# Kernel optimization log

Hardware: AMD Instinct MI355X
Metric: run time of the kernel (lower is better)

The kernel has to match this reference:

```python
import jax, jax.numpy as jnp
import numpy as np

SCALE_X = 3.0 ** 0.5  # sqrt(1 + 2*exp(highway_bias)) with highway_bias=0, rescale=True


def setup_inputs() -> dict:
    key = jax.random.key(0)
    k1, k2, k3 = jax.random.split(key, 3)
    L, B, d = 1024, 32, 512
    x = jax.random.normal(k1, (L, B, d), dtype=jnp.float32)
    # weight [n_in, 3*n_out]; scaled like xavier uniform range sqrt(3/d)
    weight = jax.random.normal(k2, (d, 3 * d), dtype=jnp.float32) * (1.0 / d) ** 0.5
    weight_c = jax.random.normal(k3, (2 * d,), dtype=jnp.float32) * 0.5
    bias = jnp.zeros((2 * d,), dtype=jnp.float32)
    c0 = jnp.zeros((B, d), dtype=jnp.float32)
    return {"x": x, "weight": weight, "weight_c": weight_c, "bias": bias, "c0": c0}


def reference(x, weight, weight_c, bias, c0):
    # x: [L, B, n_in], weight: [n_in, 3*n_out], weight_c/bias: [2*n_out], c0: [B, n_out]
    L, B, d_in = x.shape
    d = c0.shape[-1]
    # input projection GEMM: u[t,b,:] = x[t,b,:] @ W, split into (x_tilde, f_in, r_in)
    u = jnp.einsum('lbi,ik->lbk', x, weight).reshape(L, B, 3, d)
    vf, vr = weight_c[:d], weight_c[d:]
    bf, br = bias[:d], bias[d:]

    def step(c, inp):
        u_t, x_t = inp                                   # u_t: [B,3,d], x_t: [B,d]
        f = jax.nn.sigmoid(u_t[:, 1] + vf * c + bf)      # forget gate from c_{t-1}
        c_new = f * c + (1.0 - f) * u_t[:, 0]            # cell state
        r = jax.nn.sigmoid(u_t[:, 2] + vr * c_new + br)  # reset/highway gate from c_t
        g = jnp.tanh(c_new)                              # activation_type=1 (tanh)
        h = r * g + (1.0 - r) * (x_t * SCALE_X)          # highway skip (k=3: uses x*scale)
        return c_new, h

    c_last, h = jax.lax.scan(step, c0, (u, x))
    return h, c_last
```

## Files before the change

### kernel.cpp

```cpp
#include <hip/hip_runtime.h>
#include <hip/hip_bf16.h>


typedef __attribute__((ext_vector_type(8))) __bf16 bf16x8;
typedef __attribute__((ext_vector_type(4))) __bf16 bf16x4;
typedef __attribute__((ext_vector_type(4))) float floatx4;

#define WAITV(N) asm volatile("s_waitcnt vmcnt(" #N ")" ::: "memory")
#define WAITL() asm volatile("s_waitcnt lgkmcnt(0)" ::: "memory")

#define GK 512
#define GN 1536

__global__ __launch_bounds__(256) void cvt_w(const float* __restrict__ w,
                                             __bf16* __restrict__ wt) {
  __shared__ float tile[64][65];
  const int bk = blockIdx.x;
  const int bn = blockIdx.y;
  const int t = threadIdx.x;
  const int tr = t >> 6;
  const int tc = t & 63;
#pragma unroll
  for (int i = 0; i < 16; ++i) {
    int kl = i * 4 + tr;
    tile[kl][tc] = w[(size_t)(bk * 64 + kl) * GN + bn * 64 + tc];
  }
  __syncthreads();
#pragma unroll
  for (int i = 0; i < 16; ++i) {
    int nl = i * 4 + tr;
    wt[(size_t)(bn * 64 + nl) * GK + bk * 64 + tc] = (__bf16)tile[tc][nl];
  }
}

__global__ __launch_bounds__(512, 2) void fused_kernel(
    const float* __restrict__ x, const __bf16* __restrict__ wt,
    const float* __restrict__ wc, const float* __restrict__ bias,
    const float* __restrict__ c0, float* __restrict__ out) {
  __shared__ __attribute__((aligned(16))) __bf16 xbuf[2][16 * 512];
  __shared__ __attribute__((aligned(16))) float ubuf[2][16][201];
  const int g = blockIdx.x;
  const int b = (g & 7) * 4 + ((g >> 3) & 3);
  const int j0 = (g >> 5) * 64;
  const int wave = threadIdx.x >> 6;
  const int lane = threadIdx.x & 63;
  const int quad = lane >> 4, l16 = lane & 15;

  if (wave < 6) {
    const int comp = wave >> 1, hn = wave & 1;
    const int lnb = comp * 64 + hn * 32;
    const int nb = comp * 512 + j0 + hn * 32;
    bf16x8 breg[16][2];
#pragma unroll
    for (int ki = 0; ki < 16; ++ki)
#pragma unroll
      for (int nt = 0; nt < 2; ++nt)
        breg[ki][nt] = *(const bf16x8*)(wt + (size_t)(nb + nt * 16 + l16) * GK +
                                        ki * 32 + quad * 8);
    __builtin_amdgcn_s_barrier();
    for (int s = 0; s < 64; ++s) {
      const __bf16* xb = xbuf[s & 1];
      floatx4 acc0 = {}, acc1 = {};
#pragma unroll
      for (int ki = 0; ki < 16; ++ki) {
        bf16x8 af = *(const bf16x8*)(xb + l16 * 512 +
                                     (((4 * ki + quad) ^ (l16 & 7)) * 8));
        acc0 = __builtin_amdgcn_mfma_f32_16x16x32_bf16(af, breg[ki][0], acc0, 0, 0, 0);
        acc1 = __builtin_amdgcn_mfma_f32_16x16x32_bf16(af, breg[ki][1], acc1, 0, 0, 0);
      }
      float* ub = &ubuf[s & 1][0][0];
#pragma unroll
      for (int i = 0; i < 4; ++i) {
        ub[(quad * 4 + i) * 201 + lnb + l16] = acc0[i];
        ub[(quad * 4 + i) * 201 + lnb + 16 + l16] = acc1[i];
      }
      WAITL();
      __builtin_amdgcn_s_barrier();
    }
  } else if (wave == 6) {
    const float* xsrc = x + (size_t)b * 512;
    float4 xr[32];
#define XISSUE(BLK)                                                         \
  _Pragma("unroll") for (int v = 0; v < 32; ++v) {                          \
    int r = v >> 1;                                                         \
    int fq = (v & 1) * 64 + lane;                                           \
    xr[v] = *(const float4*)(xsrc + (size_t)((BLK) * 16 + r) * 16384 + fq * 4); \
  }
#define XWRITE(BUF)                                                         \
  _Pragma("unroll") for (int v = 0; v < 32; ++v) {                          \
    int r = v >> 1;                                                         \
    int fq = (v & 1) * 64 + lane;                                           \
    float4 w4 = xr[v];                                                      \
    bf16x4 o = {(__bf16)w4.x, (__bf16)w4.y, (__bf16)w4.z, (__bf16)w4.w};    \
    *(bf16x4*)((__bf16*)xbuf[BUF] + r * 512 + (((fq >> 1) ^ (r & 7)) * 8) + \
               (fq & 1) * 4) = o;                                           \
  }
    XISSUE(0);
    WAITV(0);
    XWRITE(0);
    XISSUE(1);
    WAITL();
    __builtin_amdgcn_s_barrier();
    for (int s = 0; s < 64; ++s) {
      if (s + 1 < 64) {
        WAITV(0);
        XWRITE((s + 1) & 1);
      }
      if (s + 2 < 64) XISSUE(s + 2);
      WAITL();
      __builtin_amdgcn_s_barrier();
    }
#undef XISSUE
#undef XWRITE
  } else {
    const int ob = b * 512 + j0 + lane;
    const float L2E = 1.4426950408889634f;
    const float vf = wc[j0 + lane], vr = wc[512 + j0 + lane];
    const float bfv = bias[j0 + lane], brv = bias[512 + j0 + lane];
    const float wf2 = -vf * L2E;
    const float wr2 = -vr * L2E;
    float c = c0[ob];
    float* op = out + ob;
    const float* xs2 = x + ob;
    float xa[16], xb2[16];
#define XLOAD(BANK, BLK)                                                    \
  _Pragma("unroll") for (int i = 0; i < 16; ++i) BANK[i] =                  \
      xs2[(size_t)((BLK) * 16 + i) * 16384];
#define CONSUME(S1, BANK)                                                   \
  {                                                                         \
    const float* ub = &ubuf[(S1) & 1][0][0];                                \
    float u0a[16], k2a[16], cc[16];                                         \
                        \
    _Pragma("unroll") for (int i = 0; i < 16; ++i) {                        \
      u0a[i] = ub[i * 201 + lane];                                          \
      float u1 = ub[i * 201 + 64 + lane];                                   \
      k2a[i] = -(u1 + bfv) * L2E;                                           \
    }                                                                       \
        \
    _Pragma("unroll") for (int i = 0; i < 16; ++i) {                        \
      float t = __builtin_fmaf(wf2, c, k2a[i]);                             \
      float e;                                                              \
      asm("v_exp_f32 %0, %1" : "=v"(e) : "v"(t));                           \
      float fr = __builtin_amdgcn_rcpf(1.f + e);                            \
      c = __builtin_fmaf(c - u0a[i], fr, u0a[i]);                           \
      cc[i] = c;                                                            \
    }                                                                       \
                \
    _Pragma("unroll") for (int i = 0; i < 16; ++i) {                        \
      float ci = cc[i];                                                     \
      float u2 = ub[i * 201 + 128 + lane];                                  \
      float t2 = __builtin_fmaf(wr2, ci, -(u2 + brv) * L2E);                \
      float e2;                                                             \
      asm("v_exp_f32 %0, %1" : "=v"(e2) : "v"(t2));                         \
      float rg = __builtin_amdgcn_rcpf(1.f + e2);                           \
      float t3 = __builtin_fabsf(ci) * (-2.f * L2E);                        \
      float e3;                                                             \
      asm("v_exp_f32 %0, %1" : "=v"(e3) : "v"(t3));                         \
      float gg = (1.f - e3) * __builtin_amdgcn_rcpf(1.f + e3);              \
      gg = __builtin_copysignf(gg, ci);                                     \
      float xsc = BANK[i] * 1.7320508075688772f;                            \
      float h = __builtin_fmaf(rg, gg - xsc, xsc);                          \
      op[(size_t)((S1) * 16 + i) * 16384] = h;                              \
    }                                                                       \
  }
    __builtin_amdgcn_s_barrier();
    XLOAD(xa, 0);
    __builtin_amdgcn_s_barrier();
    for (int sp = 1; sp < 63; sp += 2) {
      XLOAD(xb2, sp);
      WAITV(16);
      CONSUME(sp - 1, xa);
      __builtin_amdgcn_s_barrier();
      XLOAD(xa, sp + 1);
      WAITV(16);
      CONSUME(sp, xb2);
      __builtin_amdgcn_s_barrier();
    }
    XLOAD(xb2, 63);
    WAITV(16);
    CONSUME(62, xa);
    __builtin_amdgcn_s_barrier();
    WAITV(16);
    CONSUME(63, xb2);
    out[(size_t)16777216 + ob] = c;
#undef XLOAD
#undef CONSUME
  }
}

extern "C" void kernel_launch(void* const* d_in, const int* in_sizes, int n_in,
                              void* d_out, int out_size, void* d_ws, size_t ws_size,
                              hipStream_t stream) {
  const float* x = (const float*)d_in[0];
  const float* w = (const float*)d_in[1];
  const float* wc = (const float*)d_in[2];
  const float* bias = (const float*)d_in[3];
  const float* c0 = (const float*)d_in[4];
  float* out = (float*)d_out;

  char* ws = (char*)d_ws;
  __bf16* wt = (__bf16*)ws;

  cvt_w<<<dim3(8, 24), 256, 0, stream>>>(w, wt);
  fused_kernel<<<256, 512, 0, stream>>>(x, wt, wc, bias, c0, out);
}
```

Baseline: 204.0 us.

## Split recurrence into c-chain and output waves with three-stage pipeline

Each block shrinks from 8 to 6 waves: 3 MFMA waves, each computing 64 columns of one gate component, 1 x-loader wave, a new wave that runs only the serial c recurrence, and a final wave that computes the r gate, tanh and output from c values passed through a new LDS buffer. The u buffer becomes triple-buffered and the loop runs 66 stages, so GEMM, the c recurrence and the output stage overlap across consecutive 16-step chunks. This aims to take the exp, tanh and store work off the serial dependency chain and to allow 3 blocks per CU. In exchange it adds pipeline fill latency and LDS traffic, and doubles the B-fragment registers held by each MFMA wave.

```diff
diff --git a/kernel.cpp b/kernel.cpp
--- a/kernel.cpp
+++ b/kernel.cpp
@@ -33,51 +33,58 @@
   }
 }
 
-__global__ __launch_bounds__(512, 2) void fused_kernel(
+__global__ __launch_bounds__(384, 3) void fused_kernel(
     const float* __restrict__ x, const __bf16* __restrict__ wt,
     const float* __restrict__ wc, const float* __restrict__ bias,
     const float* __restrict__ c0, float* __restrict__ out) {
   __shared__ __attribute__((aligned(16))) __bf16 xbuf[2][16 * 512];
-  __shared__ __attribute__((aligned(16))) float ubuf[2][16][201];
+  __shared__ __attribute__((aligned(16))) float ubuf[3][16][194];
+  __shared__ __attribute__((aligned(16))) float ccbuf[2][16][64];
   const int g = blockIdx.x;
   const int b = (g & 7) * 4 + ((g >> 3) & 3);
   const int j0 = (g >> 5) * 64;
   const int wave = threadIdx.x >> 6;
   const int lane = threadIdx.x & 63;
   const int quad = lane >> 4, l16 = lane & 15;
-
-  if (wave < 6) {
-    const int comp = wave >> 1, hn = wave & 1;
-    const int lnb = comp * 64 + hn * 32;
-    const int nb = comp * 512 + j0 + hn * 32;
-    bf16x8 breg[16][2];
+  const float L2E = 1.4426950408889634f;
+
+  if (wave < 3) {
+    const int nb = wave * 512 + j0;
+    const int lnb = wave * 64;
+    bf16x8 breg[16][4];
 #pragma unroll
     for (int ki = 0; ki < 16; ++ki)
 #pragma unroll
-      for (int nt = 0; nt < 2; ++nt)
+      for (int nt = 0; nt < 4; ++nt)
         breg[ki][nt] = *(const bf16x8*)(wt + (size_t)(nb + nt * 16 + l16) * GK +
                                         ki * 32 + quad * 8);
     __builtin_amdgcn_s_barrier();
-    for (int s = 0; s < 64; ++s) {
-      const __bf16* xb = xbuf[s & 1];
-      floatx4 acc0 = {}, acc1 = {};
-#pragma unroll
-      for (int ki = 0; ki < 16; ++ki) {
-        bf16x8 af = *(const bf16x8*)(xb + l16 * 512 +
-                                     (((4 * ki + quad) ^ (l16 & 7)) * 8));
-        acc0 = __builtin_amdgcn_mfma_f32_16x16x32_bf16(af, breg[ki][0], acc0, 0, 0, 0);
-        acc1 = __builtin_amdgcn_mfma_f32_16x16x32_bf16(af, breg[ki][1], acc1, 0, 0, 0);
-      }
-      float* ub = &ubuf[s & 1][0][0];
-#pragma unroll
-      for (int i = 0; i < 4; ++i) {
-        ub[(quad * 4 + i) * 201 + lnb + l16] = acc0[i];
-        ub[(quad * 4 + i) * 201 + lnb + 16 + l16] = acc1[i];
+    int pu = 0;
+    for (int s = 0; s < 66; ++s) {
+      if (s < 64) {
+        const __bf16* xb = xbuf[s & 1];
+        floatx4 acc[4] = {};
+#pragma unroll
+        for (int ki = 0; ki < 16; ++ki) {
+          bf16x8 af = *(const bf16x8*)(xb + l16 * 512 +
+                                       (((4 * ki + quad) ^ (l16 & 7)) * 8));
+#pragma unroll
+          for (int nt = 0; nt < 4; ++nt)
+            acc[nt] = __builtin_amdgcn_mfma_f32_16x16x32_bf16(af, breg[ki][nt],
+                                                              acc[nt], 0, 0, 0);
+        }
+        float* ub = &ubuf[pu][0][0];
+#pragma unroll
+        for (int nt = 0; nt < 4; ++nt)
+#pragma unroll
+          for (int i = 0; i < 4; ++i)
+            ub[(quad * 4 + i) * 194 + lnb + nt * 16 + l16] = acc[nt][i];
+        pu = (pu == 2) ? 0 : pu + 1;
       }
       WAITL();
       __builtin_amdgcn_s_barrier();
     }
-  } else if (wave == 6) {
+  } else if (wave == 3) {
     const float* xsrc = x + (size_t)b * 512;
     float4 xr[32];
 #define XISSUE(BLK)                                                         \
@@ -101,7 +108,7 @@
     XISSUE(1);
     WAITL();
     __builtin_amdgcn_s_barrier();
-    for (int s = 0; s < 64; ++s) {
+    for (int s = 0; s < 66; ++s) {
       if (s + 1 < 64) {
         WAITV(0);
         XWRITE((s + 1) & 1);
@@ -112,43 +119,60 @@
     }
 #undef XISSUE
 #undef XWRITE
+  } else if (wave == 4) {
+    const int ob = b * 512 + j0 + lane;
+    const float vf = wc[j0 + lane], bfv = bias[j0 + lane];
+    const float wf2 = -vf * L2E;
+    float c = c0[ob];
+    __builtin_amdgcn_s_barrier();
+    int q = 0;
+    for (int s = 0; s < 66; ++s) {
+      if (s >= 1 && s <= 64) {
+        const float* ub = &ubuf[q][0][0];
+        float u0a[16], k2a[16];
+#pragma unroll
+        for (int i = 0; i < 16; ++i) {
+          u0a[i] = ub[i * 194 + lane];
+          k2a[i] = -(ub[i * 194 + 64 + lane] + bfv) * L2E;
+        }
+#pragma unroll
+        for (int i = 0; i < 16; ++i)
+          asm volatile("" : "+v"(u0a[i]), "+v"(k2a[i]));
+        __builtin_amdgcn_sched_barrier(0);
+        float* cb = &ccbuf[(s - 1) & 1][0][0];
+#pragma unroll
+        for (int i = 0; i < 16; ++i) {
+          float t = __builtin_fmaf(wf2, c, k2a[i]);
+          float e;
+          asm("v_exp_f32 %0, %1" : "=v"(e) : "v"(t));
+          float fr = __builtin_amdgcn_rcpf(1.f + e);
+          c = __builtin_fmaf(c - u0a[i], fr, u0a[i]);
+          cb[i * 64 + lane] = c;
+        }
+        q = (q == 2) ? 0 : q + 1;
+      }
+      WAITL();
+      __builtin_amdgcn_s_barrier();
+    }
   } else {
     const int ob = b * 512 + j0 + lane;
-    const float L2E = 1.4426950408889634f;
-    const float vf = wc[j0 + lane], vr = wc[512 + j0 + lane];
-    const float bfv = bias[j0 + lane], brv = bias[512 + j0 + lane];
-    const float wf2 = -vf * L2E;
+    const float vr = wc[512 + j0 + lane], brv = bias[512 + j0 + lane];
     const float wr2 = -vr * L2E;
-    float c = c0[ob];
     float* op = out + ob;
     const float* xs2 = x + ob;
-    float xa[16], xb2[16];
-#define XLOAD(BANK, BLK)                                                    \
+    float xA[16], xB[16];
+    int qp = 0;
+    __builtin_amdgcn_s_barrier();
+#define XLOADP(BANK, BLK)                                                   \
   _Pragma("unroll") for (int i = 0; i < 16; ++i) BANK[i] =                  \
       xs2[(size_t)((BLK) * 16 + i) * 16384];
-#define CONSUME(S1, BANK)                                                   \
+#define PCONS(D, BANK)                                                      \
   {                                                                         \
-    const float* ub = &ubuf[(S1) & 1][0][0];                                \
-    float u0a[16], k2a[16], cc[16];                                         \
-                        \
+    const float* ub = &ubuf[qp][0][0];                                      \
+    const float* cb = &ccbuf[(D) & 1][0][0];                                \
     _Pragma("unroll") for (int i = 0; i < 16; ++i) {                        \
-      u0a[i] = ub[i * 201 + lane];                                          \
-      float u1 = ub[i * 201 + 64 + lane];                                   \
-      k2a[i] = -(u1 + bfv) * L2E;                                           \
-    }                                                                       \
-        \
-    _Pragma("unroll") for (int i = 0; i < 16; ++i) {                        \
-      float t = __builtin_fmaf(wf2, c, k2a[i]);                             \
-      float e;                                                              \
-      asm("v_exp_f32 %0, %1" : "=v"(e) : "v"(t));                           \
-      float fr = __builtin_amdgcn_rcpf(1.f + e);                            \
-      c = __builtin_fmaf(c - u0a[i], fr, u0a[i]);                           \
-      cc[i] = c;                                                            \
-    }                                                                       \
-                \
-    _Pragma("unroll") for (int i = 0; i < 16; ++i) {                        \
-      float ci = cc[i];                                                     \
-      float u2 = ub[i * 201 + 128 + lane];                                  \
+      float ci = cb[i * 64 + lane];                                         \
+      float u2 = ub[i * 194 + 128 + lane];                                  \
       float t2 = __builtin_fmaf(wr2, ci, -(u2 + brv) * L2E);                \
       float e2;                                                             \
       asm("v_exp_f32 %0, %1" : "=v"(e2) : "v"(t2));                         \
@@ -160,31 +184,27 @@
       gg = __builtin_copysignf(gg, ci);                                     \
       float xsc = BANK[i] * 1.7320508075688772f;                            \
       float h = __builtin_fmaf(rg, gg - xsc, xsc);                          \
-      op[(size_t)((S1) * 16 + i) * 16384] = h;                              \
+      op[(size_t)((D) * 16 + i) * 16384] = h;                               \
     }                                                                       \
-  }
-    __builtin_amdgcn_s_barrier();
-    XLOAD(xa, 0);
-    __builtin_amdgcn_s_barrier();
-    for (int sp = 1; sp < 63; sp += 2) {
-      XLOAD(xb2, sp);
-      WAITV(16);
-      CONSUME(sp - 1, xa);
-      __builtin_amdgcn_s_barrier();
-      XLOAD(xa, sp + 1);
-      WAITV(16);
-      CONSUME(sp, xb2);
-      __builtin_amdgcn_s_barrier();
-    }
-    XLOAD(xb2, 63);
-    WAITV(16);
-    CONSUME(62, xa);
-    __builtin_amdgcn_s_barrier();
-    WAITV(16);
-    CONSUME(63, xb2);
-    out[(size_t)16777216 + ob] = c;
-#undef XLOAD
-#undef CONSUME
+    qp = (qp == 2) ? 0 : qp + 1;                                            \
+  }
+#define PITER(S, LB, CB)                                                    \
+  {                                                                         \
+    if ((S) >= 1 && (S) <= 64) XLOADP(LB, (S) - 1);                         \
+    if ((S) >= 2) {                                                         \
+      WAITV(16); \
+      PCONS((S) - 2, CB);                                                   \
+    }                                                                       \
+    __builtin_amdgcn_s_barrier();                                           \
+  }
+    for (int sp = 0; sp < 66; sp += 2) {
+      PITER(sp, xB, xA);
+      PITER(sp + 1, xA, xB);
+    }
+#undef XLOADP
+#undef PCONS
+#undef PITER
+    out[(size_t)16777216 + ob] = (&ccbuf[1][0][0])[15 * 64 + lane];
   }
 }
 
@@ -202,5 +222,5 @@
   __bf16* wt = (__bf16*)ws;
 
   cvt_w<<<dim3(8, 24), 256, 0, stream>>>(w, wt);
-  fused_kernel<<<256, 512, 0, stream>>>(x, wt, wc, bias, c0, out);
+  fused_kernel<<<256, 384, 0, stream>>>(x, wt, wc, bias, c0, out);
 }
```

Result: slower. 623.1 us (+205.4%).
